# Optimization experiments

Measured on AMD Instinct MI355X. Metric: run time of the kernel, lower is better.

Reference implementation:

```python
import jax, jax.numpy as jnp
import numpy as np

IN_DIM = 1024
EMBED = 512
N_PATCH = 8191  # +1 cls token -> n=8192, divisible by k-chunk 512
K_CHUNK = 512
NUM_CLASSES = 2


def setup_inputs() -> dict:
    key = jax.random.key(0)
    ks = jax.random.split(key, 16)
    g = lambda i, shape, scale=0.02: jax.random.normal(ks[i], shape, dtype=jnp.float32) * scale
    return {
        "x": jax.random.normal(ks[0], (1, N_PATCH, IN_DIM), dtype=jnp.float32),
        "W1": g(1, (IN_DIM, EMBED)), "b1": jnp.zeros((EMBED,), jnp.float32),
        "cls_token": jax.random.normal(ks[2], (1, 1, EMBED), dtype=jnp.float32),
        "Wq": g(3, (EMBED, EMBED)), "bq": jnp.zeros((EMBED,), jnp.float32),
        "Wk": g(4, (EMBED, EMBED)), "bk": jnp.zeros((EMBED,), jnp.float32),
        "Wv": g(5, (EMBED, EMBED)), "bv": jnp.zeros((EMBED,), jnp.float32),
        "Wo": g(6, (EMBED, EMBED)), "bo": jnp.zeros((EMBED,), jnp.float32),
        "ln_g": jnp.ones((EMBED,), jnp.float32), "ln_b": jnp.zeros((EMBED,), jnp.float32),
        "Wc": g(7, (EMBED, NUM_CLASSES)), "bc": jnp.zeros((NUM_CLASSES,), jnp.float32),
    }


def reference(x, W1, b1, cls_token, Wq, bq, Wk, bk, Wv, bv, Wo, bo, ln_g, ln_b, Wc, bc):
    # feature_proj: Linear -> ReLU (dropout=0 -> identity)
    h = jax.nn.relu(x @ W1 + b1)                       # [b, N, E]
    b_, _, e = h.shape
    h = jnp.concatenate([jnp.broadcast_to(cls_token, (b_, 1, e)), h], axis=1)  # prepend cls
    b, n, d = h.shape                                   # n = 8192 > 5000 path
    q = h @ Wq + bq
    k = h @ Wk + bk
    v = h @ Wv + bv
    scores = jnp.einsum("bqd,bkd->bqk", q, k) / (d ** 0.5)  # [b, n, n]
    # n>5000 branch: softmax within each K_CHUNK slice of keys, then re-softmax over full n
    w = jax.nn.softmax(scores.reshape(b, n, n // K_CHUNK, K_CHUNK), axis=-1).reshape(b, n, n)
    w = jax.nn.softmax(w, axis=-1)
    attn = jnp.einsum("bqk,bkd->bqd", w, v)
    h = h + attn @ Wo + bo                              # residual
    # LayerNorm (eps=1e-5)
    mu = h.mean(-1, keepdims=True)
    var = ((h - mu) ** 2).mean(-1, keepdims=True)
    hn = (h - mu) / jnp.sqrt(var + 1e-5) * ln_g + ln_b
    cls_feat = hn[:, 0, :]
    logits = cls_feat @ Wc + bc                         # [b, num_classes]
    return logits
```

## Files before the change

kernel.cpp:

```cpp
#include <hip/hip_runtime.h>
#include <math.h>

typedef __attribute__((ext_vector_type(8))) short bf16x8;
typedef __attribute__((ext_vector_type(4))) float f32x4;

#define AS1(p) ((__attribute__((address_space(1))) void*)(uintptr_t)(p))
#define AS3(p) ((__attribute__((address_space(3))) void*)(p))

static __device__ __forceinline__ unsigned short f2bf(float f) {
    unsigned int u = __float_as_uint(f);
    unsigned int r = (u + 0x7fffu + ((u >> 16) & 1u)) >> 16;
    return (unsigned short)r;
}

#define NPATCH 8191
#define NTOK   8192
#define INDIM  1024
#define EMBED  512

__global__ void k_pre(const float* __restrict__ x, unsigned short* __restrict__ xb,
                      const float* __restrict__ W1, unsigned short* __restrict__ w1t,
                      const float* __restrict__ cls, const float* __restrict__ Wq,
                      const float* __restrict__ bq, const float* __restrict__ bv,
                      const float* __restrict__ bo,
                      float* __restrict__ q0, float* __restrict__ h_full,
                      float* __restrict__ svec, float* __restrict__ attn0,
                      float* __restrict__ r0, float* __restrict__ scores) {
    const int b = blockIdx.x;
    const int t = threadIdx.x;
    if (b < 8) {
        __shared__ float part[4][64];
        const int c  = t >> 6;
        const int dl = t & 63;
        const int d  = b * 64 + dl;
        float acc = 0.f;
        for (int in = c; in < EMBED; in += 4)
            acc = fmaf(cls[in], Wq[(size_t)in * EMBED + d], acc);
        part[c][dl] = acc;
        __syncthreads();
        if (c == 0) {
            const float s = part[0][dl] + part[1][dl] + part[2][dl] + part[3][dl];
            q0[d]     = s + bq[d];
            h_full[d] = cls[d];
            svec[d]   = 0.f;
            attn0[d]  = bv[d];
            r0[d]     = cls[d] + bo[d];
            #pragma unroll
            for (int i = 0; i < 16; ++i) scores[d * 16 + i] = 0.f;
        }
    } else if (b < 520) {
        __shared__ float tile[32][33];
        const int bb = b - 8;
        const int bk = bb >> 4;
        const int bn = bb & 15;
        const int r  = t >> 3;
        const int c4 = (t & 7) * 4;
        float4 v = *(const float4*)(W1 + (size_t)(bk * 32 + r) * EMBED + bn * 32 + c4);
        tile[r][c4 + 0] = v.x; tile[r][c4 + 1] = v.y; tile[r][c4 + 2] = v.z; tile[r][c4 + 3] = v.w;
        __syncthreads();
        ushort4 o;
        o.x = f2bf(tile[c4 + 0][r]); o.y = f2bf(tile[c4 + 1][r]);
        o.z = f2bf(tile[c4 + 2][r]); o.w = f2bf(tile[c4 + 3][r]);
        *(ushort4*)(w1t + (size_t)(bn * 32 + r) * INDIM + bk * 32 + c4) = o;
    } else {
        const int cb = b - 520;
        const int NV = NPATCH * INDIM / 4;
        const int NT = NTOK   * INDIM / 4;
        for (int i = cb * 256 + t; i < NT; i += 2048 * 256) {
            ushort4 o;
            if (i < NV) {
                float4 v = ((const float4*)x)[i];
                o.x = f2bf(v.x); o.y = f2bf(v.y); o.z = f2bf(v.z); o.w = f2bf(v.w);
            } else {
                o.x = 0; o.y = 0; o.z = 0; o.w = 0;
            }
            ((ushort4*)xb)[i] = o;
        }
    }
}

__global__ void k_u(const float* __restrict__ Wk, const float* __restrict__ q0,
                    float* __restrict__ u) {
    const int wave = blockIdx.x * 4 + (threadIdx.x >> 6);
    const int lane = threadIdx.x & 63;
    const float4* q4 = (const float4*)q0;
    float4 qa = q4[lane * 2], qb = q4[lane * 2 + 1];
    for (int rr = 0; rr < 4; ++rr) {
        const int row = wave * 4 + rr;
        const float4* wr = (const float4*)(Wk + (size_t)row * EMBED);
        float4 a = wr[lane * 2], b = wr[lane * 2 + 1];
        float acc = a.x*qa.x + a.y*qa.y + a.z*qa.z + a.w*qa.w
                  + b.x*qb.x + b.y*qb.y + b.z*qb.z + b.w*qb.w;
        for (int off = 32; off; off >>= 1) acc += __shfl_down(acc, off);
        if (lane == 0) u[row] = acc;
    }
}

__global__ __launch_bounds__(256) void k_gemm(const unsigned short* __restrict__ xb,
                                              const unsigned short* __restrict__ w1t,
                                              const float* __restrict__ b1,
                                              const float* __restrict__ u,
                                              float* __restrict__ h_full,
                                              float* __restrict__ scores) {
    __shared__ __align__(16) unsigned short As[2][128 * 128];
    __shared__ __align__(16) unsigned short Bs[2][128 * 128];
    const int tid  = threadIdx.x;
    const int wave = tid >> 6;
    const int lane = tid & 63;
    const int bid  = blockIdx.x;
    const int rg   = (bid & 7) | ((bid >> 5) << 3);
    const int cg   = (bid >> 3) & 3;
    const int wr   = wave >> 1, wc = wave & 1;
    const int fr   = lane & 15, fq = lane >> 4;

    size_t srcA[8], srcB[8];
    int dstc[8];
    #pragma unroll
    for (int i = 0; i < 8; ++i) {
        const int c0  = (i * 4 + wave) * 64;
        const int c   = c0 + lane;
        const int row = c >> 4, koct = c & 15;
        const int kg  = koct ^ (row & 7);
        dstc[i] = c0 * 8;
        srcA[i] = (size_t)(rg * 128 + row) * INDIM + kg * 8;
        srcB[i] = (size_t)(cg * 128 + row) * INDIM + kg * 8;
    }

    f32x4 acc[4][4] = {};

    int aoff[4], boff[4];
    #pragma unroll
    for (int mi = 0; mi < 4; ++mi) {
        const int row = wr * 64 + mi * 16 + fr;
        aoff[mi] = row * 128 + ((fq ^ (row & 7)) * 8);
        const int col = wc * 64 + mi * 16 + fr;
        boff[mi] = col * 128 + ((fq ^ (col & 7)) * 8);
    }

#define STAGE(buf, k0) do { \
    _Pragma("unroll") \
    for (int i = 0; i < 8; ++i) \
        __builtin_amdgcn_global_load_lds(AS1(xb + srcA[i] + (k0)), \
                                         AS3(&As[buf][dstc[i]]), 16, 0, 0); \
    _Pragma("unroll") \
    for (int i = 0; i < 8; ++i) \
        __builtin_amdgcn_global_load_lds(AS1(w1t + srcB[i] + (k0)), \
                                         AS3(&Bs[buf][dstc[i]]), 16, 0, 0); \
    } while (0)

    STAGE(0, 0);
    __syncthreads();

    int cur = 0;
    for (int kt = 0; kt < 8; ++kt) {
        if (kt < 7) STAGE(cur ^ 1, (kt + 1) * 128);
        #pragma unroll
        for (int kk = 0; kk < 4; ++kk) {
            bf16x8 af[4], bf[4];
            #pragma unroll
            for (int mi = 0; mi < 4; ++mi)
                af[mi] = *(const bf16x8*)&As[cur][aoff[mi] ^ (kk * 32)];
            #pragma unroll
            for (int ni = 0; ni < 4; ++ni)
                bf[ni] = *(const bf16x8*)&Bs[cur][boff[ni] ^ (kk * 32)];
            #pragma unroll
            for (int mi = 0; mi < 4; ++mi)
                #pragma unroll
                for (int ni = 0; ni < 4; ++ni)
                    acc[mi][ni] = __builtin_amdgcn_mfma_f32_16x16x32_bf16(af[mi], bf[ni], acc[mi][ni], 0, 0, 0);
        }
        __syncthreads();
        cur ^= 1;
    }
#undef STAGE

    float uv[4], bvv[4];
    #pragma unroll
    for (int ni = 0; ni < 4; ++ni) {
        const int col = cg * 128 + wc * 64 + ni * 16 + fr;
        uv[ni]  = u[col];
        bvv[ni] = b1[col];
    }
    #pragma unroll
    for (int mi = 0; mi < 4; ++mi) {
        #pragma unroll
        for (int rr = 0; rr < 4; ++rr) {
            const int a = rg * 128 + wr * 64 + mi * 16 + fq * 4 + rr;
            if (a < NPATCH) {
                float sc = 0.f;
                #pragma unroll
                for (int ni = 0; ni < 4; ++ni) {
                    const int col = cg * 128 + wc * 64 + ni * 16 + fr;
                    float v = fmaxf(acc[mi][ni][rr] + bvv[ni], 0.f);
                    h_full[(size_t)(a + 1) * EMBED + col] = v;
                    sc = fmaf(v, uv[ni], sc);
                }
                sc += __shfl_xor(sc, 1);
                sc += __shfl_xor(sc, 2);
                sc += __shfl_xor(sc, 4);
                sc += __shfl_xor(sc, 8);
                if (fr == 0) atomicAdd(&scores[a + 1], sc);
            }
        }
    }
}

__global__ void k_softmax(const float* __restrict__ scores, const float* __restrict__ h_full,
                          const float* __restrict__ u, float* __restrict__ wts) {
    __shared__ float redA[16], redB[16];
    __shared__ float s0sh;
    const int t = threadIdx.x, wv = t >> 6, lane = t & 63;
    const float rs = 0.04419417382415922f;

    if (wv == 0) {
        const float4* hr = (const float4*)h_full;
        const float4* u4 = (const float4*)u;
        float4 a = hr[lane * 2], b = hr[lane * 2 + 1];
        float4 qa = u4[lane * 2], qb = u4[lane * 2 + 1];
        float acc = a.x*qa.x + a.y*qa.y + a.z*qa.z + a.w*qa.w
                  + b.x*qb.x + b.y*qb.y + b.z*qb.z + b.w*qb.w;
        for (int off = 32; off; off >>= 1) acc += __shfl_down(acc, off);
        if (lane == 0) s0sh = acc * rs;
    }
    __syncthreads();

    const float4* s4 = (const float4*)scores;
    float4 a = s4[2 * t], b = s4[2 * t + 1];
    float v[8] = {a.x*rs, a.y*rs, a.z*rs, a.w*rs, b.x*rs, b.y*rs, b.z*rs, b.w*rs};
    if (t == 0) v[0] = s0sh;

    float mx = v[0];
    #pragma unroll
    for (int j = 1; j < 8; ++j) mx = fmaxf(mx, v[j]);
    for (int off = 32; off; off >>= 1) mx = fmaxf(mx, __shfl_xor(mx, off));
    float sm = 0.f;
    #pragma unroll
    for (int j = 0; j < 8; ++j) { v[j] = expf(v[j] - mx); sm += v[j]; }
    for (int off = 32; off; off >>= 1) sm += __shfl_xor(sm, off);
    float inv = 1.f / sm;
    #pragma unroll
    for (int j = 0; j < 8; ++j) v[j] *= inv;

    float m2 = v[0];
    #pragma unroll
    for (int j = 1; j < 8; ++j) m2 = fmaxf(m2, v[j]);
    for (int off = 32; off; off >>= 1) m2 = fmaxf(m2, __shfl_xor(m2, off));
    if (lane == 0) redA[wv] = m2;
    __syncthreads();
    float gm = redA[0];
    for (int i = 1; i < 16; ++i) gm = fmaxf(gm, redA[i]);
    float s2 = 0.f;
    #pragma unroll
    for (int j = 0; j < 8; ++j) { v[j] = expf(v[j] - gm); s2 += v[j]; }
    for (int off = 32; off; off >>= 1) s2 += __shfl_xor(s2, off);
    if (lane == 0) redB[wv] = s2;
    __syncthreads();
    float gs = 0.f;
    for (int i = 0; i < 16; ++i) gs += redB[i];
    float gi = 1.f / gs;
    float4 o1 = {v[0] * gi, v[1] * gi, v[2] * gi, v[3] * gi};
    float4 o2 = {v[4] * gi, v[5] * gi, v[6] * gi, v[7] * gi};
    float4* w4 = (float4*)wts;
    w4[2 * t] = o1; w4[2 * t + 1] = o2;
}

__global__ void k_wsum(const float* __restrict__ h_full, const float* __restrict__ wts,
                       float* __restrict__ svec) {
    const int b = blockIdx.x, t = threadIdx.x;
    float a0 = 0.f, a1 = 0.f;
    const int j0 = b * 32;
    for (int j = j0; j < j0 + 32; ++j) {
        const float wj = wts[j];
        const float* hr = h_full + (size_t)j * EMBED;
        a0 = fmaf(wj, hr[t], a0);
        a1 = fmaf(wj, hr[t + 256], a1);
    }
    atomicAdd(&svec[t], a0);
    atomicAdd(&svec[t + 256], a1);
}

__global__ void k_attn0(const float* __restrict__ svec, const float* __restrict__ Wv,
                        float* __restrict__ attn0) {
    const int b = blockIdx.x, t = threadIdx.x;
    float a0 = 0.f, a1 = 0.f;
    const int e0 = b * 16;
    for (int e = e0; e < e0 + 16; ++e) {
        const float s = svec[e];
        const float* wr = Wv + (size_t)e * EMBED;
        a0 = fmaf(s, wr[t], a0);
        a1 = fmaf(s, wr[t + 256], a1);
    }
    atomicAdd(&attn0[t], a0);
    atomicAdd(&attn0[t + 256], a1);
}

__global__ void k_r0(const float* __restrict__ attn0, const float* __restrict__ Wo,
                     float* __restrict__ r0) {
    const int b = blockIdx.x, t = threadIdx.x;
    float a0 = 0.f, a1 = 0.f;
    const int e0 = b * 16;
    for (int e = e0; e < e0 + 16; ++e) {
        const float s = attn0[e];
        const float* wr = Wo + (size_t)e * EMBED;
        a0 = fmaf(s, wr[t], a0);
        a1 = fmaf(s, wr[t + 256], a1);
    }
    atomicAdd(&r0[t], a0);
    atomicAdd(&r0[t + 256], a1);
}

__global__ void k_final(const float* __restrict__ r0, const float* __restrict__ ln_g,
                        const float* __restrict__ ln_b, const float* __restrict__ Wc,
                        const float* __restrict__ bc, float* __restrict__ out) {
    __shared__ float red[8];
    const int t = threadIdx.x, wv = t >> 6, lane = t & 63;
    const float x = r0[t];

    float sm = x;
    for (int off = 32; off; off >>= 1) sm += __shfl_down(sm, off);
    if (lane == 0) red[wv] = sm;
    __syncthreads();
    float mu = 0.f;
    for (int i = 0; i < 8; ++i) mu += red[i];
    mu *= (1.f / 512.f);
    const float dx = x - mu;

    __syncthreads();
    float q = dx * dx;
    for (int off = 32; off; off >>= 1) q += __shfl_down(q, off);
    if (lane == 0) red[wv] = q;
    __syncthreads();
    float var = 0.f;
    for (int i = 0; i < 8; ++i) var += red[i];
    var *= (1.f / 512.f);

    const float hn = dx / sqrtf(var + 1e-5f) * ln_g[t] + ln_b[t];
    float p0 = hn * Wc[2 * t];
    float p1 = hn * Wc[2 * t + 1];

    __syncthreads();
    for (int off = 32; off; off >>= 1) p0 += __shfl_down(p0, off);
    if (lane == 0) red[wv] = p0;
    __syncthreads();
    if (t == 0) {
        float tot = 0.f;
        for (int i = 0; i < 8; ++i) tot += red[i];
        out[0] = tot + bc[0];
    }
    __syncthreads();
    for (int off = 32; off; off >>= 1) p1 += __shfl_down(p1, off);
    if (lane == 0) red[wv] = p1;
    __syncthreads();
    if (t == 0) {
        float tot = 0.f;
        for (int i = 0; i < 8; ++i) tot += red[i];
        out[1] = tot + bc[1];
    }
}

extern "C" void kernel_launch(void* const* d_in, const int* in_sizes, int n_in,
                              void* d_out, int out_size, void* d_ws, size_t ws_size,
                              hipStream_t stream) {
    const float* x    = (const float*)d_in[0];
    const float* W1   = (const float*)d_in[1];
    const float* b1   = (const float*)d_in[2];
    const float* cls  = (const float*)d_in[3];
    const float* Wq   = (const float*)d_in[4];
    const float* bq   = (const float*)d_in[5];
    const float* Wk   = (const float*)d_in[6];
    const float* bk   = (const float*)d_in[7];   (void)bk;
    const float* Wv   = (const float*)d_in[8];
    const float* bv   = (const float*)d_in[9];
    const float* Wo   = (const float*)d_in[10];
    const float* bo   = (const float*)d_in[11];
    const float* ln_g = (const float*)d_in[12];
    const float* ln_b = (const float*)d_in[13];
    const float* Wc   = (const float*)d_in[14];
    const float* bc   = (const float*)d_in[15];
    float* out = (float*)d_out;

    char* ws = (char*)d_ws;
    unsigned short* xb     = (unsigned short*)(ws);
    unsigned short* w1t    = (unsigned short*)(ws + 16777216);
    float*          h_full = (float*)(ws + 17825792);
    float*          scores = (float*)(ws + 34603008);
    float*          wts    = (float*)(ws + 34635776);
    float*          q0     = (float*)(ws + 34668544);
    float*          u      = (float*)(ws + 34670592);
    float*          svec   = (float*)(ws + 34672640);
    float*          attn0  = (float*)(ws + 34674688);
    float*          r0     = (float*)(ws + 34676736);

    k_pre     <<<2568, 256, 0, stream>>>(x, xb, W1, w1t, cls, Wq, bq, bv, bo,
                                         q0, h_full, svec, attn0, r0, scores);
    k_u       <<<32,  256, 0, stream>>>(Wk, q0, u);
    k_gemm    <<<256, 256, 0, stream>>>(xb, w1t, b1, u, h_full, scores);
    k_softmax <<<1,  1024, 0, stream>>>(scores, h_full, u, wts);
    k_wsum    <<<256, 256, 0, stream>>>(h_full, wts, svec);
    k_attn0   <<<32,  256, 0, stream>>>(svec, Wv, attn0);
    k_r0      <<<32,  256, 0, stream>>>(attn0, Wo, r0);
    k_final   <<<1,   512, 0, stream>>>(r0, ln_g, ln_b, Wc, bc, out);
}
```

Before: 188.0 us.

## Fuse softmax into weighted-sum kernel and restructure bf16 conversion of x

Removes the single-block 1024-thread softmax kernel. Every one of the 256 wsum blocks now recomputes the full two-stage softmax redundantly with 256 threads, each handling 32 scores, using fast __expf. It keeps only its own 32 weights in shared memory, which drops one launch and the wts round trip. The x-to-bf16 conversion in k_pre now uses 1024 blocks, each issuing eight float4 loads before converting, instead of a grid-stride loop, and the k_pre grid shrinks from 2568 to 1544 blocks. The trade-off is redundant softmax work in every block, and __expf is slightly less precise than expf.

Result: no change. 185.1 us (-1.6%).

```diff
diff --git a/kernel.cpp b/kernel.cpp
--- a/kernel.cpp
+++ b/kernel.cpp
@@ -48,9 +48,29 @@
             #pragma unroll
             for (int i = 0; i < 16; ++i) scores[d * 16 + i] = 0.f;
         }
-    } else if (b < 520) {
+    } else if (b < 1032) {
+        const int cb   = b - 8;
+        const int base = cb * 2048 + t;
+        const int NV   = NPATCH * INDIM / 4;
+        const float4* x4 = (const float4*)x;
+        ushort4* xb4 = (ushort4*)xb;
+        float4 vv[8];
+        #pragma unroll
+        for (int k = 0; k < 8; ++k) {
+            const int i = base + k * 256;
+            if (i < NV) vv[k] = x4[i];
+            else        vv[k] = make_float4(0.f, 0.f, 0.f, 0.f);
+        }
+        #pragma unroll
+        for (int k = 0; k < 8; ++k) {
+            ushort4 o;
+            o.x = f2bf(vv[k].x); o.y = f2bf(vv[k].y);
+            o.z = f2bf(vv[k].z); o.w = f2bf(vv[k].w);
+            xb4[base + k * 256] = o;
+        }
+    } else {
         __shared__ float tile[32][33];
-        const int bb = b - 8;
+        const int bb = b - 1032;
         const int bk = bb >> 4;
         const int bn = bb & 15;
         const int r  = t >> 3;
@@ -62,20 +82,6 @@
         o.x = f2bf(tile[c4 + 0][r]); o.y = f2bf(tile[c4 + 1][r]);
         o.z = f2bf(tile[c4 + 2][r]); o.w = f2bf(tile[c4 + 3][r]);
         *(ushort4*)(w1t + (size_t)(bn * 32 + r) * INDIM + bk * 32 + c4) = o;
-    } else {
-        const int cb = b - 520;
-        const int NV = NPATCH * INDIM / 4;
-        const int NT = NTOK   * INDIM / 4;
-        for (int i = cb * 256 + t; i < NT; i += 2048 * 256) {
-            ushort4 o;
-            if (i < NV) {
-                float4 v = ((const float4*)x)[i];
-                o.x = f2bf(v.x); o.y = f2bf(v.y); o.z = f2bf(v.z); o.w = f2bf(v.w);
-            } else {
-                o.x = 0; o.y = 0; o.z = 0; o.w = 0;
-            }
-            ((ushort4*)xb)[i] = o;
-        }
     }
 }
 
@@ -205,73 +211,76 @@
     }
 }
 
-__global__ void k_softmax(const float* __restrict__ scores, const float* __restrict__ h_full,
-                          const float* __restrict__ u, float* __restrict__ wts) {
-    __shared__ float redA[16], redB[16];
-    __shared__ float s0sh;
-    const int t = threadIdx.x, wv = t >> 6, lane = t & 63;
+__global__ void k_wsum(const float* __restrict__ scores, const float* __restrict__ h_full,
+                       const float* __restrict__ u, const float* __restrict__ cls,
+                       float* __restrict__ svec) {
+    __shared__ float redf[4];
+    __shared__ float wloc[32];
+    const int b = blockIdx.x, t = threadIdx.x;
+    const int wv = t >> 6, lane = t & 63;
     const float rs = 0.04419417382415922f;
 
-    if (wv == 0) {
-        const float4* hr = (const float4*)h_full;
-        const float4* u4 = (const float4*)u;
-        float4 a = hr[lane * 2], b = hr[lane * 2 + 1];
-        float4 qa = u4[lane * 2], qb = u4[lane * 2 + 1];
-        float acc = a.x*qa.x + a.y*qa.y + a.z*qa.z + a.w*qa.w
-                  + b.x*qb.x + b.y*qb.y + b.z*qb.z + b.w*qb.w;
-        for (int off = 32; off; off >>= 1) acc += __shfl_down(acc, off);
-        if (lane == 0) s0sh = acc * rs;
-    }
-    __syncthreads();
-
-    const float4* s4 = (const float4*)scores;
-    float4 a = s4[2 * t], b = s4[2 * t + 1];
-    float v[8] = {a.x*rs, a.y*rs, a.z*rs, a.w*rs, b.x*rs, b.y*rs, b.z*rs, b.w*rs};
-    if (t == 0) v[0] = s0sh;
+    float part = cls[t] * u[t] + cls[t + 256] * u[t + 256];
+    for (int off = 32; off; off >>= 1) part += __shfl_down(part, off);
+    if (lane == 0) redf[wv] = part;
+    __syncthreads();
+    const float s0 = (redf[0] + redf[1] + redf[2] + redf[3]) * rs;
+    __syncthreads();
+
+    float v[32];
+    const float4* s4 = (const float4*)(scores + t * 32);
+    #pragma unroll
+    for (int q = 0; q < 8; ++q) {
+        float4 a = s4[q];
+        v[q*4+0] = a.x*rs; v[q*4+1] = a.y*rs; v[q*4+2] = a.z*rs; v[q*4+3] = a.w*rs;
+    }
+    if (t == 0) v[0] = s0;
 
     float mx = v[0];
     #pragma unroll
-    for (int j = 1; j < 8; ++j) mx = fmaxf(mx, v[j]);
-    for (int off = 32; off; off >>= 1) mx = fmaxf(mx, __shfl_xor(mx, off));
+    for (int j = 1; j < 32; ++j) mx = fmaxf(mx, v[j]);
+    mx = fmaxf(mx, __shfl_xor(mx, 1));
+    mx = fmaxf(mx, __shfl_xor(mx, 2));
+    mx = fmaxf(mx, __shfl_xor(mx, 4));
+    mx = fmaxf(mx, __shfl_xor(mx, 8));
     float sm = 0.f;
     #pragma unroll
-    for (int j = 0; j < 8; ++j) { v[j] = expf(v[j] - mx); sm += v[j]; }
-    for (int off = 32; off; off >>= 1) sm += __shfl_xor(sm, off);
-    float inv = 1.f / sm;
-    #pragma unroll
-    for (int j = 0; j < 8; ++j) v[j] *= inv;
+    for (int j = 0; j < 32; ++j) { v[j] = __expf(v[j] - mx); sm += v[j]; }
+    sm += __shfl_xor(sm, 1);
+    sm += __shfl_xor(sm, 2);
+    sm += __shfl_xor(sm, 4);
+    sm += __shfl_xor(sm, 8);
+    const float inv = 1.f / sm;
+    #pragma unroll
+    for (int j = 0; j < 32; ++j) v[j] *= inv;
 
     float m2 = v[0];
     #pragma unroll
-    for (int j = 1; j < 8; ++j) m2 = fmaxf(m2, v[j]);
+    for (int j = 1; j < 32; ++j) m2 = fmaxf(m2, v[j]);
     for (int off = 32; off; off >>= 1) m2 = fmaxf(m2, __shfl_xor(m2, off));
-    if (lane == 0) redA[wv] = m2;
-    __syncthreads();
-    float gm = redA[0];
-    for (int i = 1; i < 16; ++i) gm = fmaxf(gm, redA[i]);
+    if (lane == 0) redf[wv] = m2;
+    __syncthreads();
+    const float gm = fmaxf(fmaxf(redf[0], redf[1]), fmaxf(redf[2], redf[3]));
+    __syncthreads();
     float s2 = 0.f;
     #pragma unroll
-    for (int j = 0; j < 8; ++j) { v[j] = expf(v[j] - gm); s2 += v[j]; }
+    for (int j = 0; j < 32; ++j) { v[j] = __expf(v[j] - gm); s2 += v[j]; }
     for (int off = 32; off; off >>= 1) s2 += __shfl_xor(s2, off);
-    if (lane == 0) redB[wv] = s2;
-    __syncthreads();
-    float gs = 0.f;
-    for (int i = 0; i < 16; ++i) gs += redB[i];
-    float gi = 1.f / gs;
-    float4 o1 = {v[0] * gi, v[1] * gi, v[2] * gi, v[3] * gi};
-    float4 o2 = {v[4] * gi, v[5] * gi, v[6] * gi, v[7] * gi};
-    float4* w4 = (float4*)wts;
-    w4[2 * t] = o1; w4[2 * t + 1] = o2;
-}
-
-__global__ void k_wsum(const float* __restrict__ h_full, const float* __restrict__ wts,
-                       float* __restrict__ svec) {
-    const int b = blockIdx.x, t = threadIdx.x;
+    if (lane == 0) redf[wv] = s2;
+    __syncthreads();
+    const float gi = 1.f / (redf[0] + redf[1] + redf[2] + redf[3]);
+
+    if (t == b) {
+        #pragma unroll
+        for (int j = 0; j < 32; ++j) wloc[j] = v[j] * gi;
+    }
+    __syncthreads();
+
     float a0 = 0.f, a1 = 0.f;
-    const int j0 = b * 32;
-    for (int j = j0; j < j0 + 32; ++j) {
-        const float wj = wts[j];
-        const float* hr = h_full + (size_t)j * EMBED;
+    #pragma unroll 4
+    for (int j = 0; j < 32; ++j) {
+        const float wj = wloc[j];
+        const float* hr = h_full + (size_t)(b * 32 + j) * EMBED;
         a0 = fmaf(wj, hr[t], a0);
         a1 = fmaf(wj, hr[t + 256], a1);
     }
@@ -384,20 +393,18 @@
     unsigned short* w1t    = (unsigned short*)(ws + 16777216);
     float*          h_full = (float*)(ws + 17825792);
     float*          scores = (float*)(ws + 34603008);
-    float*          wts    = (float*)(ws + 34635776);
     float*          q0     = (float*)(ws + 34668544);
     float*          u      = (float*)(ws + 34670592);
     float*          svec   = (float*)(ws + 34672640);
     float*          attn0  = (float*)(ws + 34674688);
     float*          r0     = (float*)(ws + 34676736);
 
-    k_pre     <<<2568, 256, 0, stream>>>(x, xb, W1, w1t, cls, Wq, bq, bv, bo,
-                                         q0, h_full, svec, attn0, r0, scores);
-    k_u       <<<32,  256, 0, stream>>>(Wk, q0, u);
-    k_gemm    <<<256, 256, 0, stream>>>(xb, w1t, b1, u, h_full, scores);
-    k_softmax <<<1,  1024, 0, stream>>>(scores, h_full, u, wts);
-    k_wsum    <<<256, 256, 0, stream>>>(h_full, wts, svec);
-    k_attn0   <<<32,  256, 0, stream>>>(svec, Wv, attn0);
-    k_r0      <<<32,  256, 0, stream>>>(attn0, Wo, r0);
-    k_final   <<<1,   512, 0, stream>>>(r0, ln_g, ln_b, Wc, bc, out);
-}
+    k_pre   <<<1544, 256, 0, stream>>>(x, xb, W1, w1t, cls, Wq, bq, bv, bo,
+                                       q0, h_full, svec, attn0, r0, scores);
+    k_u     <<<32,   256, 0, stream>>>(Wk, q0, u);
+    k_gemm  <<<256,  256, 0, stream>>>(xb, w1t, b1, u, h_full, scores);
+    k_wsum  <<<256,  256, 0, stream>>>(scores, h_full, u, cls, svec);
+    k_attn0 <<<32,   256, 0, stream>>>(svec, Wv, attn0);
+    k_r0    <<<32,   256, 0, stream>>>(attn0, Wo, r0);
+    k_final <<<1,    512, 0, stream>>>(r0, ln_g, ln_b, Wc, bc, out);
+}
```
